# Kernel optimization log

Measured on AMD Instinct MI355X. Metric: run time of the kernel, lower is better.

The kernel has to match this reference:

```python
import jax, jax.numpy as jnp
import numpy as np

DIVIDE = 1.0


def setup_inputs() -> dict:
    key = jax.random.key(0)
    ks = jax.random.split(key, 12)
    B, NH, L, H, DIM = 2, 8, 1024, 64, 64
    return {
        "mask": jax.random.normal(ks[0], (B, NH, L, L), dtype=jnp.float32),
        "q": jax.random.normal(ks[1], (B, L, NH, H), dtype=jnp.float32),
        "k": jax.random.normal(ks[2], (B, L, NH, H), dtype=jnp.float32),
        "v": jax.random.normal(ks[3], (B, L, NH, H), dtype=jnp.float32),
        "W0": jax.random.normal(ks[4], (1, DIM), dtype=jnp.float32) * 0.02,
        "b0": jnp.zeros((DIM,), dtype=jnp.float32),
        "W1": jax.random.normal(ks[5], (DIM, DIM), dtype=jnp.float32) * 0.02,
        "b1": jnp.zeros((DIM,), dtype=jnp.float32),
        "W2": jax.random.normal(ks[6], (DIM, DIM), dtype=jnp.float32) * 0.02,
        "b2": jnp.zeros((DIM,), dtype=jnp.float32),
        "Wf": jax.random.normal(ks[7], (DIM, 8), dtype=jnp.float32) * 0.02,
        "bf": jnp.zeros((8,), dtype=jnp.float32),
    }


def reference(mask, q, k, v, W0, b0, W1, b1, W2, b2, Wf, bf):
    # default positions: arange over L1 / L2; identical across batch so we
    # compute the (L1, L2) relative-position grid once and broadcast.
    L1, L2 = q.shape[-3], k.shape[-3]
    pos_q = jnp.arange(L1, dtype=q.dtype)
    pos_k = jnp.arange(L2, dtype=q.dtype)
    rel = (pos_q[:, None] - pos_k[None, :]) / DIVIDE          # (L1, L2)
    rel = rel[..., None]                                       # (L1, L2, 1)
    # depth-3 MLP: Linear -> SiLU (norm=False => Identity), final Linear to n_heads
    h = jax.nn.silu(rel @ W0 + b0)                             # (L1, L2, DIM)
    h = jax.nn.silu(h @ W1 + b1)
    h = jax.nn.silu(h @ W2 + b2)
    bias = h @ Wf + bf                                         # (L1, L2, NH)
    bias = jnp.moveaxis(bias, -1, 0)                           # (NH, L1, L2)
    # mask shapes already match q/k lengths -> no padding branch needed
    return mask - bias                                          # broadcast over B
```

## Files before the change

kernel.cpp:

```cpp
#include <hip/hip_runtime.h>
#include <hip/hip_bf16.h>


#define L_SEQ 1024
#define NDIAG (2 * L_SEQ - 1)
#define NH 8
#define DIM 64

__device__ __forceinline__ float silu_f(float x) {
    return x / (1.0f + __expf(-x));
}

__global__ __launch_bounds__(DIM) void build_bias_table(
    const float* __restrict__ W0, const float* __restrict__ b0,
    const float* __restrict__ W1, const float* __restrict__ b1,
    const float* __restrict__ W2, const float* __restrict__ b2,
    const float* __restrict__ Wf, const float* __restrict__ bf,
    float* __restrict__ tab ) {
    const int d = blockIdx.x;
    const int t = threadIdx.x;
    const float rel = (float)(d - (L_SEQ - 1));

    __shared__ float sh[DIM];

    float h = silu_f(rel * W0[t] + b0[t]);
    sh[t] = h;
    __syncthreads();

    float acc = b1[t];
    #pragma unroll
    for (int k = 0; k < DIM; ++k) acc += sh[k] * W1[k * DIM + t];
    float h1 = silu_f(acc);
    __syncthreads();
    sh[t] = h1;
    __syncthreads();

    acc = b2[t];
    #pragma unroll
    for (int k = 0; k < DIM; ++k) acc += sh[k] * W2[k * DIM + t];
    float h2 = silu_f(acc);
    __syncthreads();
    sh[t] = h2;
    __syncthreads();

    if (t < NH) {
        float a = bf[t];
        #pragma unroll
        for (int k = 0; k < DIM; ++k) a += sh[k] * Wf[k * NH + t];
        tab[t * NDIAG + d] = a;
    }
}

__global__ __launch_bounds__(256) void apply_bias(
    const float4* __restrict__ mask, const float* __restrict__ tab,
    float4* __restrict__ out, int n4) {
    int idx = blockIdx.x * blockDim.x + threadIdx.x;
    const int stride = gridDim.x * blockDim.x;
    for (; idx < n4; idx += stride) {
        const int n = idx << 2;
        const int j = n & (L_SEQ - 1);
        const int i = (n >> 10) & (L_SEQ - 1);
        const int h = (n >> 20) & (NH - 1);
        const float* tb = tab + h * NDIAG + (i - j + (L_SEQ - 1));
        const float4 m = mask[idx];
        float4 o;
        o.x = m.x - tb[0];
        o.y = m.y - tb[-1];
        o.z = m.z - tb[-2];
        o.w = m.w - tb[-3];
        out[idx] = o;
    }
}

extern "C" void kernel_launch(void* const* d_in, const int* in_sizes, int n_in,
                              void* d_out, int out_size, void* d_ws, size_t ws_size,
                              hipStream_t stream) {
    const float* mask = (const float*)d_in[0];
    const float* W0 = (const float*)d_in[4];
    const float* b0 = (const float*)d_in[5];
    const float* W1 = (const float*)d_in[6];
    const float* b1 = (const float*)d_in[7];
    const float* W2 = (const float*)d_in[8];
    const float* b2 = (const float*)d_in[9];
    const float* Wf = (const float*)d_in[10];
    const float* bf = (const float*)d_in[11];
    float* out = (float*)d_out;

    float* tab = (float*)d_ws;

    build_bias_table<<<NDIAG, DIM, 0, stream>>>(W0, b0, W1, b1, W2, b2, Wf, bf, tab);

    const int n4 = out_size / 4;
    const int block = 256;
    const int grid = 2048;
    apply_bias<<<grid, block, 0, stream>>>(
        (const float4*)mask, tab, (float4*)out, n4);
}
```

Measured before the change: 31.63 us.

## Pack four diagonals per table block; nontemporal streaming and fixed grid in apply

After: 32.96 us. 4.2% more time.

```diff
diff --git a/kernel.cpp b/kernel.cpp
--- a/kernel.cpp
+++ b/kernel.cpp
@@ -7,68 +7,73 @@
 #define NH 8
 #define DIM 64
 
+typedef float f32x4 __attribute__((ext_vector_type(4)));
+
 __device__ __forceinline__ float silu_f(float x) {
     return x / (1.0f + __expf(-x));
 }
 
-__global__ __launch_bounds__(DIM) void build_bias_table(
+__global__ __launch_bounds__(256) void build_bias_table(
     const float* __restrict__ W0, const float* __restrict__ b0,
     const float* __restrict__ W1, const float* __restrict__ b1,
     const float* __restrict__ W2, const float* __restrict__ b2,
     const float* __restrict__ Wf, const float* __restrict__ bf,
     float* __restrict__ tab ) {
-    const int d = blockIdx.x;
-    const int t = threadIdx.x;
+    const int g = threadIdx.x >> 6;
+    const int t = threadIdx.x & 63;
+    const int d = blockIdx.x * 4 + g;
     const float rel = (float)(d - (L_SEQ - 1));
 
-    __shared__ float sh[DIM];
+    __shared__ float sh[4][DIM];
 
     float h = silu_f(rel * W0[t] + b0[t]);
-    sh[t] = h;
+    sh[g][t] = h;
     __syncthreads();
 
     float acc = b1[t];
     #pragma unroll
-    for (int k = 0; k < DIM; ++k) acc += sh[k] * W1[k * DIM + t];
+    for (int k = 0; k < DIM; ++k) acc += sh[g][k] * W1[k * DIM + t];
     float h1 = silu_f(acc);
     __syncthreads();
-    sh[t] = h1;
+    sh[g][t] = h1;
     __syncthreads();
 
     acc = b2[t];
     #pragma unroll
-    for (int k = 0; k < DIM; ++k) acc += sh[k] * W2[k * DIM + t];
+    for (int k = 0; k < DIM; ++k) acc += sh[g][k] * W2[k * DIM + t];
     float h2 = silu_f(acc);
     __syncthreads();
-    sh[t] = h2;
+    sh[g][t] = h2;
     __syncthreads();
 
-    if (t < NH) {
+    if (t < NH && d < NDIAG) {
         float a = bf[t];
         #pragma unroll
-        for (int k = 0; k < DIM; ++k) a += sh[k] * Wf[k * NH + t];
+        for (int k = 0; k < DIM; ++k) a += sh[g][k] * Wf[k * NH + t];
         tab[t * NDIAG + d] = a;
     }
 }
 
 __global__ __launch_bounds__(256) void apply_bias(
-    const float4* __restrict__ mask, const float* __restrict__ tab,
-    float4* __restrict__ out, int n4) {
-    int idx = blockIdx.x * blockDim.x + threadIdx.x;
-    const int stride = gridDim.x * blockDim.x;
-    for (; idx < n4; idx += stride) {
-        const int n = idx << 2;
+    const f32x4* __restrict__ mask, const float* __restrict__ tab,
+    f32x4* __restrict__ out, int half4) {
+    const int idx = blockIdx.x * 256 + threadIdx.x;
+
+    #pragma unroll
+    for (int p = 0; p < 2; ++p) {
+        const int id = idx + p * half4;
+        const int n = id << 2;
         const int j = n & (L_SEQ - 1);
         const int i = (n >> 10) & (L_SEQ - 1);
         const int h = (n >> 20) & (NH - 1);
         const float* tb = tab + h * NDIAG + (i - j + (L_SEQ - 1));
-        const float4 m = mask[idx];
-        float4 o;
+        const f32x4 m = __builtin_nontemporal_load(&mask[id]);
+        f32x4 o;
         o.x = m.x - tb[0];
         o.y = m.y - tb[-1];
         o.z = m.z - tb[-2];
         o.w = m.w - tb[-3];
-        out[idx] = o;
+        __builtin_nontemporal_store(o, &out[id]);
     }
 }
 
@@ -88,11 +93,12 @@
 
     float* tab = (float*)d_ws;
 
-    build_bias_table<<<NDIAG, DIM, 0, stream>>>(W0, b0, W1, b1, W2, b2, Wf, bf, tab);
+    build_bias_table<<<(NDIAG + 3) / 4, 256, 0, stream>>>(
+        W0, b0, W1, b1, W2, b2, Wf, bf, tab);
 
     const int n4 = out_size / 4;
-    const int block = 256;
-    const int grid = 2048;
-    apply_bias<<<grid, block, 0, stream>>>(
-        (const float4*)mask, tab, (float4*)out, n4);
+    const int half4 = n4 / 2;
+    const int grid = half4 / 256;
+    apply_bias<<<grid, 256, 0, stream>>>(
+        (const f32x4*)mask, tab, (f32x4*)out, half4);
 }
```
